# Kernel optimization log

Measured on AMD Instinct MI355X. Metric: run time of the kernel, lower is better.

## Reference

```python
import jax, jax.numpy as jnp
import numpy as np
from jax.ops import segment_sum

NEG_SLOPE = 0.2
N0, N1, N2, N3 = 100000, 300000, 150000, 50000
DIN, DMID = 64, 128


def setup_inputs() -> dict:
    key = jax.random.key(0)
    ks = jax.random.split(key, 16)
    g = lambda k, shp, fan_in: jax.random.normal(k, shp, dtype=jnp.float32) * (1.0 / np.sqrt(fan_in))
    return {
        "x_0": jax.random.normal(ks[0], (N0, DIN), dtype=jnp.float32),
        "x_1": jax.random.normal(ks[1], (N1, DIN), dtype=jnp.float32),
        "x_2": jax.random.normal(ks[2], (N2, DIN), dtype=jnp.float32),
        "x_3": jax.random.normal(ks[3], (N3, DIN), dtype=jnp.float32),
        "x_4": jax.random.normal(ks[4], (10000, DIN), dtype=jnp.float32),
        # COO indices: row 0 = destination (row of sparse matrix), row 1 = source (column)
        "adj0_idx": jax.random.randint(ks[5], (2, 800000), 0, N0),
        "adj3_idx": jax.random.randint(ks[6], (2, 800000), 0, N3),
        "inc01_t": jax.random.randint(ks[7], (600000,), 0, N0),   # rows of incidence_0_1 (0-cells)
        "inc01_s": jax.random.randint(ks[8], (600000,), 0, N1),   # cols (1-cells)
        "inc23_t": jax.random.randint(ks[9], (200000,), 0, N2),   # rows of incidence_2_3 (2-cells)
        "inc23_s": jax.random.randint(ks[10], (200000,), 0, N3),  # cols (3-cells)
        "W_hbs0": g(ks[11], (DIN, DMID), DIN),
        "W_hbs3": g(ks[12], (DIN, DMID), DIN),
        "W_s01": g(ks[13], (DIN, DMID), DIN),   # HBNS source weight: x_1 -> target-rank (0) messages
        "W_t23": g(ks[14], (DIN, DMID), DIN),   # HBNS target weight: x_2 -> source-rank (3) messages
        "fc0_W": g(ks[15], (DMID, DMID), DMID),
        "fc0_b": jnp.zeros((DMID,), dtype=jnp.float32),
        "fc3_W": g(jax.random.fold_in(key, 100), (DMID, DMID), DMID),
        "fc3_b": jnp.zeros((DMID,), dtype=jnp.float32),
    }


def _spmm(msg, dst, src, n_out):
    # out[i] = sum_{(i,j) in nnz} msg[j]  == sparse_matrix @ msg
    return segment_sum(msg[src], dst, num_segments=n_out)


def reference(x_0, x_1, x_2, x_3, x_4, adj0_idx, adj3_idx, inc01_t, inc01_s,
              inc23_t, inc23_s, W_hbs0, W_hbs3, W_s01, W_t23,
              fc0_W, fc0_b, fc3_W, fc3_b):
    lrelu = lambda v: jax.nn.leaky_relu(v, NEG_SLOPE)
    # HBS within-rank propagation: A @ (x W)
    x_0_to_0 = _spmm(x_0 @ W_hbs0, adj0_idx[0], adj0_idx[1], x_0.shape[0])
    x_3_to_3 = _spmm(x_3 @ W_hbs3, adj3_idx[0], adj3_idx[1], x_3.shape[0])
    # HBNS cross-rank propagation
    # message on target rank 0: incidence_0_1 @ (x_1 W_s)
    x_1_to_0 = _spmm(x_1 @ W_s01, inc01_t, inc01_s, x_0.shape[0])
    # message on source rank 3: incidence_2_3^T @ (x_2 W_t)
    x_2_to_3 = _spmm(x_2 @ W_t23, inc23_s, inc23_t, x_3.shape[0])
    # sum aggregation + FC + LeakyReLU
    x_0_new = lrelu((x_0_to_0 + x_1_to_0) @ fc0_W.T + fc0_b)
    x_3_new = lrelu((x_2_to_3 + x_3_to_3) @ fc3_W.T + fc3_b)
    return (x_0_new, x_1, x_2, x_3_new, x_4)
```

## Files before the change

### kernel.cpp

```cpp
#include <hip/hip_runtime.h>

#define NEG_SLOPE 0.2f
#define NPART 16


__global__ __launch_bounds__(256) void hist_all(const int* __restrict__ ad0,
                                                const int* __restrict__ d1,
                                                const int* __restrict__ ad3,
                                                const int* __restrict__ d2,
                                                int E0, int E01, int E3, int E23,
                                                int n0, int n3,
                                                int* __restrict__ counts) {
    int T = E0 + E01 + E3 + E23;
    int i = blockIdx.x * 256 + threadIdx.x;
    int stride = gridDim.x * 256;
    for (; i < T; i += stride) {
        int j = i, d, base;
        if (j < E0) { d = ad0[j]; base = 0; }
        else if ((j -= E0) < E01) { d = d1[j]; base = n0; }
        else if ((j -= E01) < E3) { d = ad3[j]; base = 2 * n0; }
        else { j -= E3; d = d2[j]; base = 2 * n0 + n3; }
        atomicAdd(&counts[base + d], 1);
    }
}

__global__ __launch_bounds__(256) void chunk_sum(const int* __restrict__ counts,
                                                 int* __restrict__ bsum, int NT) {
    __shared__ int red[256];
    int base = blockIdx.x * 2048;
    int t = threadIdx.x;
    int s = 0;
#pragma unroll
    for (int j = 0; j < 8; ++j) {
        int idx = base + j * 256 + t;
        if (idx < NT) s += counts[idx];
    }
    red[t] = s;
    __syncthreads();
    for (int off = 128; off > 0; off >>= 1) {
        if (t < off) red[t] += red[t + off];
        __syncthreads();
    }
    if (t == 0) bsum[blockIdx.x] = red[0];
}

__global__ __launch_bounds__(256) void scan_bsum(const int* __restrict__ bsum,
                                                 int* __restrict__ bbase, int nb) {
    __shared__ int sh[256];
    int t = threadIdx.x;
    int v = (t < nb) ? bsum[t] : 0;
    sh[t] = v;
    __syncthreads();
    for (int off = 1; off < 256; off <<= 1) {
        int add = (t >= off) ? sh[t - off] : 0;
        __syncthreads();
        sh[t] += add;
        __syncthreads();
    }
    if (t < nb) bbase[t] = sh[t] - v;
}

__global__ __launch_bounds__(256) void chunk_scan(const int* __restrict__ counts,
                                                  const int* __restrict__ bbase,
                                                  int* __restrict__ offsets,
                                                  int* __restrict__ cursors,
                                                  int NT, int E_total) {
    __shared__ int tsum[256];
    int t = threadIdx.x;
    int base = blockIdx.x * 2048 + t * 8;
    int v[8];
    int s = 0;
#pragma unroll
    for (int j = 0; j < 8; ++j) {
        int idx = base + j;
        v[j] = (idx < NT) ? counts[idx] : 0;
        s += v[j];
    }
    tsum[t] = s;
    __syncthreads();
    for (int off = 1; off < 256; off <<= 1) {
        int add = (t >= off) ? tsum[t - off] : 0;
        __syncthreads();
        tsum[t] += add;
        __syncthreads();
    }
    int run = bbase[blockIdx.x] + tsum[t] - s;
#pragma unroll
    for (int j = 0; j < 8; ++j) {
        int idx = base + j;
        if (idx < NT) { offsets[idx] = run; cursors[idx] = run; }
        run += v[j];
    }
    if (blockIdx.x == 0 && t == 0) offsets[NT] = E_total;
}

__global__ __launch_bounds__(256) void fill_part(const int* __restrict__ ad0,
                                                 const int* __restrict__ as0,
                                                 const int* __restrict__ d1,
                                                 const int* __restrict__ s1,
                                                 const int* __restrict__ ad3,
                                                 const int* __restrict__ as3,
                                                 const int* __restrict__ d2,
                                                 const int* __restrict__ s2,
                                                 int E0, int E01, int E3, int E23,
                                                 int n0, int n3, int PS,
                                                 int* __restrict__ cursors,
                                                 int* __restrict__ edge_src) {
    int T = E0 + E01 + E3 + E23;
    int p = blockIdx.x & (NPART - 1);
    int bp = blockIdx.x / NPART;
    int nbp = gridDim.x / NPART;
    int lo = p * PS, hi = lo + PS;
    int stride = nbp * 256;
    for (int i = bp * 256 + threadIdx.x; i < T; i += stride) {
        int j = i, d, base;
        if (j < E0) { d = ad0[j]; base = 0; }
        else if ((j -= E0) < E01) { d = d1[j]; base = n0; }
        else if ((j -= E01) < E3) { d = ad3[j]; base = 2 * n0; }
        else { j -= E3; d = d2[j]; base = 2 * n0 + n3; }
        int cd = base + d;
        if (cd >= lo && cd < hi) {
            int s;
            int jj = i;
            if (jj < E0) s = as0[jj];
            else if ((jj -= E0) < E01) s = s1[jj];
            else if ((jj -= E01) < E3) s = as3[jj];
            else { jj -= E3; s = s2[jj]; }
            int pos = atomicAdd(&cursors[cd], 1);
            edge_src[pos] = s;
        }
    }
}

__global__ __launch_bounds__(256) void gather4(const int* __restrict__ offsets,
                                               const int* __restrict__ edge_src,
                                               const float* __restrict__ x0,
                                               const float* __restrict__ x1,
                                               const float* __restrict__ x2,
                                               const float* __restrict__ x3,
                                               float* __restrict__ agg0,
                                               float* __restrict__ agg3,
                                               int n0, int n3) {
    const int NT = 2 * n0 + 2 * n3;
    int row = blockIdx.x * 16 + (threadIdx.x >> 4);
    int c4 = (threadIdx.x & 15) * 4;
    if (row >= NT) return;
    const float* xs;
    float* outp;
    if (row < n0)               { xs = x0; outp = &agg0[(size_t)row * 128]; }
    else if (row < 2 * n0)      { xs = x1; outp = &agg0[(size_t)(row - n0) * 128 + 64]; }
    else if (row < 2 * n0 + n3) { xs = x3; outp = &agg3[(size_t)(row - 2 * n0) * 128]; }
    else                        { xs = x2; outp = &agg3[(size_t)(row - 2 * n0 - n3) * 128 + 64]; }

    int k = offsets[row], end = offsets[row + 1];
    float4 acc = make_float4(0.f, 0.f, 0.f, 0.f);
    for (; k + 2 <= end; k += 2) {
        int i0 = edge_src[k];
        int i1 = edge_src[k + 1];
        float4 a = *(const float4*)&xs[(size_t)i0 * 64 + c4];
        float4 b = *(const float4*)&xs[(size_t)i1 * 64 + c4];
        acc.x += a.x + b.x;
        acc.y += a.y + b.y;
        acc.z += a.z + b.z;
        acc.w += a.w + b.w;
    }
    if (k < end) {
        int i0 = edge_src[k];
        float4 a = *(const float4*)&xs[(size_t)i0 * 64 + c4];
        acc.x += a.x; acc.y += a.y; acc.z += a.z; acc.w += a.w;
    }
    *(float4*)&outp[c4] = acc;
}

__global__ __launch_bounds__(256) void combine_w2(const float* __restrict__ Wtop0,
                                                  const float* __restrict__ Wbot0,
                                                  const float* __restrict__ F0,
                                                  float* __restrict__ WC0,
                                                  const float* __restrict__ Wtop3,
                                                  const float* __restrict__ Wbot3,
                                                  const float* __restrict__ F3,
                                                  float* __restrict__ WC3) {
    int gi = blockIdx.x * 256 + threadIdx.x;
    int which = gi >> 14;
    int i = gi & 16383;
    const float* Wtop = which ? Wtop3 : Wtop0;
    const float* Wbot = which ? Wbot3 : Wbot0;
    const float* F = which ? F3 : F0;
    float* WC = which ? WC3 : WC0;
    int k = i >> 7;
    int c = i & 127;
    const float* wrow = (k < 64) ? &Wtop[(size_t)k * 128] : &Wbot[(size_t)(k - 64) * 128];
    const float* frow = &F[(size_t)c * 128];
    float s = 0.f;
#pragma unroll 8
    for (int j = 0; j < 128; j += 4) {
        float4 w = *(const float4*)&wrow[j];
        float4 f = *(const float4*)&frow[j];
        s = fmaf(w.x, f.x, s);
        s = fmaf(w.y, f.y, s);
        s = fmaf(w.z, f.z, s);
        s = fmaf(w.w, f.w, s);
    }
    WC[(size_t)k * 128 + c] = s;
}

__global__ __launch_bounds__(256) void fc_lrelu(const float* __restrict__ A,
                                                const float* __restrict__ WC,
                                                const float* __restrict__ bias,
                                                float* __restrict__ Y, int n) {
    __shared__ float WS[64][128];
    __shared__ float XS[64][68];
    const int t = threadIdx.x;
    const int row0 = blockIdx.x * 64;
    const int c = (t & 31) * 4;
    const int rbase = (t >> 5) * 8;
    float acc[8][4];
#pragma unroll
    for (int i = 0; i < 8; ++i)
#pragma unroll
        for (int j = 0; j < 4; ++j) acc[i][j] = 0.f;

    for (int p = 0; p < 2; ++p) {
        __syncthreads();
        const float4* Wp4 = (const float4*)(WC + (size_t)p * 64 * 128);
        float4* WS4 = (float4*)&WS[0][0];
        for (int i = t; i < 2048; i += 256) WS4[i] = Wp4[i];
        for (int i = t; i < 64 * 16; i += 256) {
            int r = i >> 4, c4 = i & 15;
            float4 v = make_float4(0.f, 0.f, 0.f, 0.f);
            if (row0 + r < n)
                v = *(const float4*)&A[(size_t)(row0 + r) * 128 + p * 64 + c4 * 4];
            *(float4*)&XS[r][c4 * 4] = v;
        }
        __syncthreads();

#pragma unroll 4
        for (int k = 0; k < 64; k += 4) {
            float4 w[4];
            w[0] = *(const float4*)&WS[k + 0][c];
            w[1] = *(const float4*)&WS[k + 1][c];
            w[2] = *(const float4*)&WS[k + 2][c];
            w[3] = *(const float4*)&WS[k + 3][c];
#pragma unroll
            for (int i = 0; i < 8; ++i) {
                float4 x = *(const float4*)&XS[rbase + i][k];
                float xs[4] = {x.x, x.y, x.z, x.w};
#pragma unroll
                for (int kk = 0; kk < 4; ++kk) {
                    acc[i][0] = fmaf(xs[kk], w[kk].x, acc[i][0]);
                    acc[i][1] = fmaf(xs[kk], w[kk].y, acc[i][1]);
                    acc[i][2] = fmaf(xs[kk], w[kk].z, acc[i][2]);
                    acc[i][3] = fmaf(xs[kk], w[kk].w, acc[i][3]);
                }
            }
        }
    }

    float4 b = *(const float4*)&bias[c];
    float bs[4] = {b.x, b.y, b.z, b.w};
#pragma unroll
    for (int i = 0; i < 8; ++i) {
        int r = row0 + rbase + i;
        if (r < n) {
            float o[4];
#pragma unroll
            for (int j = 0; j < 4; ++j) {
                float v = acc[i][j] + bs[j];
                o[j] = v > 0.f ? v : NEG_SLOPE * v;
            }
            *(float4*)&Y[(size_t)r * 128 + c] = make_float4(o[0], o[1], o[2], o[3]);
        }
    }
}

__global__ __launch_bounds__(256) void copy_all(const float4* __restrict__ s1, float4* __restrict__ o1, int m1,
                                                const float4* __restrict__ s2, float4* __restrict__ o2, int m2,
                                                const float4* __restrict__ s4, float4* __restrict__ o4, int m4) {
    int total = m1 + m2 + m4;
    int i = blockIdx.x * 256 + threadIdx.x;
    int stride = gridDim.x * 256;
    for (; i < total; i += stride) {
        int j = i;
        if (j < m1) { o1[j] = s1[j]; }
        else if ((j -= m1) < m2) { o2[j] = s2[j]; }
        else { j -= m2; o4[j] = s4[j]; }
    }
}

extern "C" void kernel_launch(void* const* d_in, const int* in_sizes, int n_in,
                              void* d_out, int out_size, void* d_ws, size_t ws_size,
                              hipStream_t stream) {
    const float* x0 = (const float*)d_in[0];
    const float* x1 = (const float*)d_in[1];
    const float* x2 = (const float*)d_in[2];
    const float* x3 = (const float*)d_in[3];
    const float* x4 = (const float*)d_in[4];
    const int* adj0 = (const int*)d_in[5];
    const int* adj3 = (const int*)d_in[6];
    const int* inc01_t = (const int*)d_in[7];
    const int* inc01_s = (const int*)d_in[8];
    const int* inc23_t = (const int*)d_in[9];
    const int* inc23_s = (const int*)d_in[10];
    const float* W_hbs0 = (const float*)d_in[11];
    const float* W_hbs3 = (const float*)d_in[12];
    const float* W_s01 = (const float*)d_in[13];
    const float* W_t23 = (const float*)d_in[14];
    const float* fc0_W = (const float*)d_in[15];
    const float* fc0_b = (const float*)d_in[16];
    const float* fc3_W = (const float*)d_in[17];
    const float* fc3_b = (const float*)d_in[18];

    const int n0 = in_sizes[0] / 64, n1 = in_sizes[1] / 64;
    const int n2 = in_sizes[2] / 64, n3 = in_sizes[3] / 64, n4 = in_sizes[4] / 64;
    const int E0 = in_sizes[5] / 2, E3 = in_sizes[6] / 2;
    const int E01 = in_sizes[7], E23 = in_sizes[9];
    const int NT = 2 * n0 + 2 * n3;
    const int E_total = E0 + E01 + E3 + E23;
    const int nb = (NT + 2047) / 2048;
    const int PS = (NT + NPART - 1) / NPART;

    float* ws = (float*)d_ws;
    size_t off = 0;
    float* agg0 = ws + off; off += (size_t)n0 * 128;
    float* agg3 = ws + off; off += (size_t)n3 * 128;
    float* wc0 = ws + off;  off += 16384;
    float* wc3 = ws + off;  off += 16384;
    int* counts = (int*)(ws + off);   off += NT;
    int* offsets = (int*)(ws + off);  off += NT + 1;
    int* cursors = (int*)(ws + off);  off += NT;
    int* bsum = (int*)(ws + off);     off += 256;
    int* bbase = (int*)(ws + off);    off += 256;
    int* edge_src = (int*)(ws + off); off += E_total;

    float* out = (float*)d_out;
    float* o_x0 = out;
    float* o_x1 = o_x0 + (size_t)n0 * 128;
    float* o_x2 = o_x1 + (size_t)n1 * 64;
    float* o_x3 = o_x2 + (size_t)n2 * 64;
    float* o_x4 = o_x3 + (size_t)n3 * 128;

    hipMemsetAsync(counts, 0, (size_t)NT * sizeof(int), stream);
    hist_all<<<(E_total + 255) / 256, 256, 0, stream>>>(
        adj0, inc01_t, adj3, inc23_s, E0, E01, E3, E23, n0, n3, counts);
    chunk_sum<<<nb, 256, 0, stream>>>(counts, bsum, NT);
    scan_bsum<<<1, 256, 0, stream>>>(bsum, bbase, nb);
    chunk_scan<<<nb, 256, 0, stream>>>(counts, bbase, offsets, cursors, NT, E_total);
    fill_part<<<NPART * 256, 256, 0, stream>>>(
        adj0, adj0 + E0, inc01_t, inc01_s, adj3, adj3 + E3, inc23_s, inc23_t,
        E0, E01, E3, E23, n0, n3, PS, cursors, edge_src);

    gather4<<<(NT + 15) / 16, 256, 0, stream>>>(offsets, edge_src, x0, x1, x2, x3,
                                                agg0, agg3, n0, n3);

    combine_w2<<<128, 256, 0, stream>>>(W_hbs0, W_s01, fc0_W, wc0,
                                        W_hbs3, W_t23, fc3_W, wc3);
    fc_lrelu<<<(n0 + 63) / 64, 256, 0, stream>>>(agg0, wc0, fc0_b, o_x0, n0);
    fc_lrelu<<<(n3 + 63) / 64, 256, 0, stream>>>(agg3, wc3, fc3_b, o_x3, n3);

    copy_all<<<8192, 256, 0, stream>>>((const float4*)x1, (float4*)o_x1, n1 * 16,
                                       (const float4*)x2, (float4*)o_x2, n2 * 16,
                                       (const float4*)x4, (float4*)o_x4, n4 * 16);
}
```

Baseline: 726.3 us.

## Pre-bin edges into destination-range buckets before histogram and CSR fill

Replaces the global histogram and the partitioned fill with a two-level binning scheme. Edges are first scattered into 16 coarse buckets by destination high bits, with shared-memory counting and one global reservation per block. The per-node histogram and CSR fill then read only their own bucket, so each launch touches a localized range of the counts and cursors arrays. The old fill kernel had every partition re-read all edges; this removes that redundant read at the cost of an extra int2 bucket buffer and two extra small kernels.

```diff
diff --git a/kernel.cpp b/kernel.cpp
--- a/kernel.cpp
+++ b/kernel.cpp
@@ -1,27 +1,116 @@
 #include <hip/hip_runtime.h>
 
 #define NEG_SLOPE 0.2f
-#define NPART 16
-
-
-__global__ __launch_bounds__(256) void hist_all(const int* __restrict__ ad0,
-                                                const int* __restrict__ d1,
-                                                const int* __restrict__ ad3,
-                                                const int* __restrict__ d2,
-                                                int E0, int E01, int E3, int E23,
-                                                int n0, int n3,
-                                                int* __restrict__ counts) {
+#define PSHIFT 15
+#define MAXP 16
+#define EPB 2048
+
+
+__device__ __forceinline__ int decode_dst(int j, const int* ad0, const int* d1,
+                                          const int* ad3, const int* d2,
+                                          int E0, int E01, int E3,
+                                          int n0, int n3) {
+    if (j < E0) return ad0[j];
+    if ((j -= E0) < E01) return n0 + d1[j];
+    if ((j -= E01) < E3) return 2 * n0 + ad3[j];
+    return 2 * n0 + n3 + d2[j - E3];
+}
+
+__device__ __forceinline__ int decode_src(int j, const int* as0, const int* s1,
+                                          const int* as3, const int* s2,
+                                          int E0, int E01, int E3) {
+    if (j < E0) return as0[j];
+    if ((j -= E0) < E01) return s1[j];
+    if ((j -= E01) < E3) return as3[j];
+    return s2[j - E3];
+}
+
+__global__ __launch_bounds__(256) void bin_sizes(const int* __restrict__ ad0,
+                                                 const int* __restrict__ d1,
+                                                 const int* __restrict__ ad3,
+                                                 const int* __restrict__ d2,
+                                                 int E0, int E01, int E3, int E23,
+                                                 int n0, int n3,
+                                                 int* __restrict__ gsizes) {
+    __shared__ int h[MAXP];
+    if (threadIdx.x < MAXP) h[threadIdx.x] = 0;
+    __syncthreads();
     int T = E0 + E01 + E3 + E23;
-    int i = blockIdx.x * 256 + threadIdx.x;
     int stride = gridDim.x * 256;
-    for (; i < T; i += stride) {
-        int j = i, d, base;
-        if (j < E0) { d = ad0[j]; base = 0; }
-        else if ((j -= E0) < E01) { d = d1[j]; base = n0; }
-        else if ((j -= E01) < E3) { d = ad3[j]; base = 2 * n0; }
-        else { j -= E3; d = d2[j]; base = 2 * n0 + n3; }
-        atomicAdd(&counts[base + d], 1);
-    }
+    for (int i = blockIdx.x * 256 + threadIdx.x; i < T; i += stride) {
+        int cd = decode_dst(i, ad0, d1, ad3, d2, E0, E01, E3, n0, n3);
+        atomicAdd(&h[cd >> PSHIFT], 1);
+    }
+    __syncthreads();
+    if (threadIdx.x < MAXP) atomicAdd(&gsizes[threadIdx.x], h[threadIdx.x]);
+}
+
+__global__ void scan16(const int* __restrict__ gsizes,
+                       int* __restrict__ pstart, int* __restrict__ bcursor) {
+    if (threadIdx.x == 0 && blockIdx.x == 0) {
+        int run = 0;
+        for (int p = 0; p < MAXP; ++p) {
+            pstart[p] = run;
+            bcursor[p] = run;
+            run += gsizes[p];
+        }
+        pstart[MAXP] = run;
+    }
+}
+
+__global__ __launch_bounds__(256) void bin_scatter(const int* __restrict__ ad0,
+                                                   const int* __restrict__ as0,
+                                                   const int* __restrict__ d1,
+                                                   const int* __restrict__ s1,
+                                                   const int* __restrict__ ad3,
+                                                   const int* __restrict__ as3,
+                                                   const int* __restrict__ d2,
+                                                   const int* __restrict__ s2,
+                                                   int E0, int E01, int E3, int E23,
+                                                   int n0, int n3,
+                                                   int* __restrict__ bcursor,
+                                                   int2* __restrict__ bucket) {
+    __shared__ int h[MAXP], base[MAXP], loc[MAXP];
+    int t = threadIdx.x;
+    if (t < MAXP) { h[t] = 0; loc[t] = 0; }
+    __syncthreads();
+
+    int T = E0 + E01 + E3 + E23;
+    int b0 = blockIdx.x * EPB;
+    int cd[EPB / 256], sv[EPB / 256];
+    bool ok[EPB / 256];
+#pragma unroll
+    for (int j = 0; j < EPB / 256; ++j) {
+        int idx = b0 + j * 256 + t;
+        ok[j] = idx < T;
+        if (ok[j]) {
+            cd[j] = decode_dst(idx, ad0, d1, ad3, d2, E0, E01, E3, n0, n3);
+            sv[j] = decode_src(idx, as0, s1, as3, s2, E0, E01, E3);
+            atomicAdd(&h[cd[j] >> PSHIFT], 1);
+        }
+    }
+    __syncthreads();
+    if (t < MAXP && h[t] > 0) base[t] = atomicAdd(&bcursor[t], h[t]);
+    __syncthreads();
+#pragma unroll
+    for (int j = 0; j < EPB / 256; ++j) {
+        if (ok[j]) {
+            int p = cd[j] >> PSHIFT;
+            int o = atomicAdd(&loc[p], 1);
+            bucket[base[p] + o] = make_int2(cd[j], sv[j]);
+        }
+    }
+}
+
+__global__ __launch_bounds__(256) void hist_part(const int2* __restrict__ bucket,
+                                                 const int* __restrict__ pstart,
+                                                 int* __restrict__ counts, int BPC) {
+    int p = blockIdx.x & (MAXP - 1);
+    int r = blockIdx.x >> 4;
+    int beg = pstart[p], end = pstart[p + 1];
+    int stride = BPC * 256;
+    for (int i = beg + r * 256 + (int)threadIdx.x; i < end; i += stride)
+        atomicAdd(&counts[bucket[i].x], 1);
 }
 
 __global__ __launch_bounds__(256) void chunk_sum(const int* __restrict__ counts,
@@ -94,41 +183,18 @@
     if (blockIdx.x == 0 && t == 0) offsets[NT] = E_total;
 }
 
-__global__ __launch_bounds__(256) void fill_part(const int* __restrict__ ad0,
-                                                 const int* __restrict__ as0,
-                                                 const int* __restrict__ d1,
-                                                 const int* __restrict__ s1,
-                                                 const int* __restrict__ ad3,
-                                                 const int* __restrict__ as3,
-                                                 const int* __restrict__ d2,
-                                                 const int* __restrict__ s2,
-                                                 int E0, int E01, int E3, int E23,
-                                                 int n0, int n3, int PS,
+__global__ __launch_bounds__(256) void part_fill(const int2* __restrict__ bucket,
+                                                 const int* __restrict__ pstart,
                                                  int* __restrict__ cursors,
-                                                 int* __restrict__ edge_src) {
-    int T = E0 + E01 + E3 + E23;
-    int p = blockIdx.x & (NPART - 1);
-    int bp = blockIdx.x / NPART;
-    int nbp = gridDim.x / NPART;
-    int lo = p * PS, hi = lo + PS;
-    int stride = nbp * 256;
-    for (int i = bp * 256 + threadIdx.x; i < T; i += stride) {
-        int j = i, d, base;
-        if (j < E0) { d = ad0[j]; base = 0; }
-        else if ((j -= E0) < E01) { d = d1[j]; base = n0; }
-        else if ((j -= E01) < E3) { d = ad3[j]; base = 2 * n0; }
-        else { j -= E3; d = d2[j]; base = 2 * n0 + n3; }
-        int cd = base + d;
-        if (cd >= lo && cd < hi) {
-            int s;
-            int jj = i;
-            if (jj < E0) s = as0[jj];
-            else if ((jj -= E0) < E01) s = s1[jj];
-            else if ((jj -= E01) < E3) s = as3[jj];
-            else { jj -= E3; s = s2[jj]; }
-            int pos = atomicAdd(&cursors[cd], 1);
-            edge_src[pos] = s;
-        }
+                                                 int* __restrict__ edge_src, int BPC) {
+    int p = blockIdx.x & (MAXP - 1);
+    int r = blockIdx.x >> 4;
+    int beg = pstart[p], end = pstart[p + 1];
+    int stride = BPC * 256;
+    for (int i = beg + r * 256 + (int)threadIdx.x; i < end; i += stride) {
+        int2 e = bucket[i];
+        int pos = atomicAdd(&cursors[e.x], 1);
+        edge_src[pos] = e.y;
     }
 }
 
@@ -317,7 +383,7 @@
     const int NT = 2 * n0 + 2 * n3;
     const int E_total = E0 + E01 + E3 + E23;
     const int nb = (NT + 2047) / 2048;
-    const int PS = (NT + NPART - 1) / NPART;
+    const int BPC = 64;
 
     float* ws = (float*)d_ws;
     size_t off = 0;
@@ -326,10 +392,15 @@
     float* wc0 = ws + off;  off += 16384;
     float* wc3 = ws + off;  off += 16384;
     int* counts = (int*)(ws + off);   off += NT;
+    int* gsizes = (int*)(ws + off);   off += MAXP;
     int* offsets = (int*)(ws + off);  off += NT + 1;
     int* cursors = (int*)(ws + off);  off += NT;
     int* bsum = (int*)(ws + off);     off += 256;
     int* bbase = (int*)(ws + off);    off += 256;
+    int* pstart = (int*)(ws + off);   off += MAXP + 1;
+    int* bcursor = (int*)(ws + off);  off += MAXP;
+    off = (off + 1) & ~(size_t)1;
+    int2* bucket = (int2*)(ws + off); off += (size_t)E_total * 2;
     int* edge_src = (int*)(ws + off); off += E_total;
 
     float* out = (float*)d_out;
@@ -339,15 +410,18 @@
     float* o_x3 = o_x2 + (size_t)n2 * 64;
     float* o_x4 = o_x3 + (size_t)n3 * 128;
 
-    hipMemsetAsync(counts, 0, (size_t)NT * sizeof(int), stream);
-    hist_all<<<(E_total + 255) / 256, 256, 0, stream>>>(
-        adj0, inc01_t, adj3, inc23_s, E0, E01, E3, E23, n0, n3, counts);
+    hipMemsetAsync(counts, 0, (size_t)(NT + MAXP) * sizeof(int), stream);
+    bin_sizes<<<2048, 256, 0, stream>>>(adj0, inc01_t, adj3, inc23_s,
+                                        E0, E01, E3, E23, n0, n3, gsizes);
+    scan16<<<1, 64, 0, stream>>>(gsizes, pstart, bcursor);
+    bin_scatter<<<(E_total + EPB - 1) / EPB, 256, 0, stream>>>(
+        adj0, adj0 + E0, inc01_t, inc01_s, adj3, adj3 + E3, inc23_s, inc23_t,
+        E0, E01, E3, E23, n0, n3, bcursor, bucket);
+    hist_part<<<MAXP * BPC, 256, 0, stream>>>(bucket, pstart, counts, BPC);
     chunk_sum<<<nb, 256, 0, stream>>>(counts, bsum, NT);
     scan_bsum<<<1, 256, 0, stream>>>(bsum, bbase, nb);
     chunk_scan<<<nb, 256, 0, stream>>>(counts, bbase, offsets, cursors, NT, E_total);
-    fill_part<<<NPART * 256, 256, 0, stream>>>(
-        adj0, adj0 + E0, inc01_t, inc01_s, adj3, adj3 + E3, inc23_s, inc23_t,
-        E0, E01, E3, E23, n0, n3, PS, cursors, edge_src);
+    part_fill<<<MAXP * BPC, 256, 0, stream>>>(bucket, pstart, cursors, edge_src, BPC);
 
     gather4<<<(NT + 15) / 16, 256, 0, stream>>>(offsets, edge_src, x0, x1, x2, x3,
                                                 agg0, agg3, n0, n3);
```

Measured after the change: 809.1 us. 11.4% more time.
